# Optimization experiments

Measured on AMD Instinct MI355X. Metric: run time of the kernel, lower is better.

Reference implementation:

```python
import jax, jax.numpy as jnp
import numpy as np

DIM = 768
NUM_HEADS = 12
DECAY_RATE = 5.0


def setup_inputs() -> dict:
    key = jax.random.key(0)
    k1, k2, k3, k4 = jax.random.split(key, 4)
    B, N, C = 4, 1024, DIM
    x = jax.random.normal(k1, (B, N, C), dtype=jnp.float32)
    # torch nn.Linear weights: y = x @ W.T ; qkv_bias=False
    qkv_w = jax.random.normal(k2, (3 * C, C), dtype=jnp.float32) * (1.0 / np.sqrt(C))
    proj_w = jax.random.normal(k3, (C, C), dtype=jnp.float32) * (1.0 / np.sqrt(C))
    proj_b = jax.random.normal(k4, (C,), dtype=jnp.float32) * 0.01
    return {"x": x, "qkv_w": qkv_w, "proj_w": proj_w, "proj_b": proj_b, "cur_epoch": 3}


def reference(x, qkv_w, proj_w, proj_b, cur_epoch):
    B, N, C = x.shape
    H = NUM_HEADS
    hd = C // H
    scale = hd ** -0.5

    qkv = (x @ qkv_w.T).reshape(B, N, 3, H, hd).transpose(2, 0, 3, 1, 4)  # [3,B,H,N,hd]
    q, k, v = qkv[0], qkv[1], qkv[2]

    scores = jnp.einsum("bhqd,bhkd->bhqk", q, k) * scale
    logp = jax.nn.log_softmax(scores, axis=-1)
    attn = jnp.exp(logp)  # [B,H,N,N]

    # Per-key entropy: column j of attn flattened over (B,H,N) is renormalized
    # by Categorical; dividing by num_heads cancels under normalization.
    # H(p/s) = log(s) - (1/s) * sum(p * log p)
    s = jnp.sum(attn, axis=(0, 1, 2))                 # [N]
    plogp = jnp.sum(attn * logp, axis=(0, 1, 2))      # [N]
    entropies = jnp.log(s) - plogp / s

    # threshold decay: factor = sum_{i=0}^{cur_epoch-1} decay*exp(-(i+1))
    factor = DECAY_RATE * float(np.sum(np.exp(-(np.arange(cur_epoch) + 1.0))))
    entropy_threshold = float(np.log(C)) - factor

    # attn[:,:,:,keep] @ v[:,:,keep,:] == (attn * mask) @ v  (zeroed columns drop out)
    mask = (entropies <= entropy_threshold).astype(attn.dtype)  # [N]
    out = jnp.einsum("bhqk,bhkd->bhqd", attn * mask[None, None, None, :], v)
    out = out.transpose(0, 2, 1, 3).reshape(B, N, C)
    out = out @ proj_w.T + proj_b
    return out
```

## Files before the change

kernel.cpp:

```cpp
#include <hip/hip_runtime.h>


typedef __bf16 bf16x8 __attribute__((ext_vector_type(8)));
typedef __bf16 bf16x4 __attribute__((ext_vector_type(4)));
typedef float  f32x4  __attribute__((ext_vector_type(4)));

#define MFMA16(a, b, c) __builtin_amdgcn_mfma_f32_16x16x32_bf16((a), (b), (c), 0, 0, 0)
#define QSCALE 0.18033688f
#define LN2    0.69314718f

__device__ __forceinline__ void ld_glds16(const __bf16* g, __bf16* s) {
  __builtin_amdgcn_global_load_lds(
      (const __attribute__((address_space(1))) unsigned int*)g,
      (__attribute__((address_space(3))) unsigned int*)s, 16, 0, 0);
}

__global__ __launch_bounds__(256) void kc_conv(
    const float* __restrict__ x, const float* __restrict__ qw, const float* __restrict__ pw,
    __bf16* __restrict__ xb, __bf16* __restrict__ qwb, __bf16* __restrict__ pwb,
    float* __restrict__ colSP, int* __restrict__ keepCnt)
{
  const int i = blockIdx.x * 256 + threadIdx.x;
  const float4* src;
  __bf16* dst;
  int j;
  if (i < 786432)       { src = (const float4*)x;  dst = xb;  j = i; }
  else if (i < 1228800) { src = (const float4*)qw; dst = qwb; j = i - 786432; }
  else                  { src = (const float4*)pw; dst = pwb; j = i - 1228800; }
  const float4 f = src[j];
  bf16x4 o;
  o[0] = (__bf16)f.x; o[1] = (__bf16)f.y; o[2] = (__bf16)f.z; o[3] = (__bf16)f.w;
  *(bf16x4*)(dst + 4 * (size_t)j) = o;
  if (i < 2048) colSP[i] = 0.f;
  if (i == 0) *keepCnt = 0;
}

__global__ __launch_bounds__(256) void kg_qkv(
    const __bf16* __restrict__ A, const __bf16* __restrict__ Bm,
    __bf16* __restrict__ qb, __bf16* __restrict__ kb, float* __restrict__ v)
{
  __shared__ __bf16 As[128 * 64];
  __shared__ __bf16 Bs[128 * 64];
  const int tid = threadIdx.x;
  const int w = tid >> 6, lane = tid & 63, quad = lane >> 4, l = lane & 15;
  const int wm = w >> 1, wn = w & 1;
  const int r0 = blockIdx.y * 128, c0 = blockIdx.x * 128;
  const int srow = lane >> 3, skk = (lane & 7) * 8;

  f32x4 acc[4][4] = {};

  for (int k0 = 0; k0 < 768; k0 += 64) {
    if (k0) __syncthreads();
#pragma unroll
    for (int s = 0; s < 4; ++s) {
      const int si = w * 4 + s;
      const int row = si * 8 + srow;
      ld_glds16(A + (size_t)(r0 + row) * 768 + k0 + skk, &As[si * 512]);
      ld_glds16(Bm + (size_t)(c0 + row) * 768 + k0 + skk, &Bs[si * 512]);
    }
    __syncthreads();
#pragma unroll
    for (int kk = 0; kk < 2; ++kk) {
      bf16x8 af[4], bf[4];
#pragma unroll
      for (int t = 0; t < 4; ++t) {
        af[t] = *(const bf16x8*)&As[(wm * 64 + t * 16 + l) * 64 + kk * 32 + quad * 8];
        bf[t] = *(const bf16x8*)&Bs[(wn * 64 + t * 16 + l) * 64 + kk * 32 + quad * 8];
      }
#pragma unroll
      for (int mt = 0; mt < 4; ++mt)
#pragma unroll
        for (int nt = 0; nt < 4; ++nt)
          acc[mt][nt] = MFMA16(af[mt], bf[nt], acc[mt][nt]);
    }
  }

  const int part = c0 / 768;
  const int cbase = c0 % 768;
#pragma unroll
  for (int mt = 0; mt < 4; ++mt) {
#pragma unroll
    for (int nt = 0; nt < 4; ++nt) {
      const int cc = cbase + wn * 64 + nt * 16 + l;
      const int h = cc >> 6, d = cc & 63;
#pragma unroll
      for (int i = 0; i < 4; ++i) {
        const int rg = r0 + wm * 64 + mt * 16 + quad * 4 + i;
        const int b_ = rg >> 10, n = rg & 1023;
        const size_t off = ((size_t)(b_ * 12 + h) * 1024 + n) * 64 + d;
        const float val = acc[mt][nt][i];
        if (part == 0)      qb[off] = (__bf16)(val * QSCALE);
        else if (part == 1) kb[off] = (__bf16)val;
        else                v[off]  = val;
      }
    }
  }
}

__global__ __launch_bounds__(512) void ks_fused(
    const __bf16* __restrict__ qb, const __bf16* __restrict__ kb,
    float* __restrict__ lse, float* __restrict__ colSP)
{
  __shared__ float sS[1024];
  __shared__ float sP[1024];
  __shared__ float zrow[64];
  const int tid = threadIdx.x;
  const int w = tid >> 6, lane = tid & 63, quad = lane >> 4, l = lane & 15;
  const int bh = blockIdx.x, r0 = blockIdx.y * 64;
  for (int i = tid; i < 1024; i += 512) { sS[i] = 0.f; sP[i] = 0.f; }
  if (tid < 64) zrow[tid] = 0.f;
  __syncthreads();

  const __bf16* qbase = qb + ((size_t)bh * 1024 + r0 + l) * 64;
  bf16x8 aq0[4], aq1[4];
#pragma unroll
  for (int rt = 0; rt < 4; ++rt) {
    aq0[rt] = *(const bf16x8*)(qbase + rt * 1024 + quad * 8);
    aq1[rt] = *(const bf16x8*)(qbase + rt * 1024 + 32 + quad * 8);
  }
  const __bf16* kfrag = kb + (size_t)bh * 65536 + (size_t)(w * 16 + l) * 64 + quad * 8;
  const f32x4 zero = {0.f, 0.f, 0.f, 0.f};

  bf16x8 kf0 = *(const bf16x8*)(kfrag);
  bf16x8 kf1 = *(const bf16x8*)(kfrag + 32);

  float z[16] = {};
  for (int s = 0; s < 8; ++s) {
    const bf16x8 c0 = kf0, c1 = kf1;
    const int nxt = (s + 1) & 7;
    kf0 = *(const bf16x8*)(kfrag + (size_t)nxt * 8192);
    kf1 = *(const bf16x8*)(kfrag + (size_t)nxt * 8192 + 32);
    f32x4 av[4];
#pragma unroll
    for (int rt = 0; rt < 4; ++rt) {
      av[rt] = MFMA16(aq0[rt], c0, zero);
      av[rt] = MFMA16(aq1[rt], c1, av[rt]);
    }
#pragma unroll
    for (int rt = 0; rt < 4; ++rt)
#pragma unroll
      for (int r = 0; r < 4; ++r) z[rt * 4 + r] += exp2f(av[rt][r]);
  }
#pragma unroll
  for (int off = 1; off < 16; off <<= 1) {
#pragma unroll
    for (int i = 0; i < 16; ++i) z[i] += __shfl_xor(z[i], off);
  }
  if (l == 0) {
#pragma unroll
    for (int rt = 0; rt < 4; ++rt)
#pragma unroll
      for (int r = 0; r < 4; ++r)
        atomicAdd(&zrow[rt * 16 + quad * 4 + r], z[rt * 4 + r]);
  }
  __syncthreads();
  if (tid < 64) lse[bh * 1024 + r0 + tid] = __log2f(zrow[tid]);
  float nlb[16];
#pragma unroll
  for (int rt = 0; rt < 4; ++rt)
#pragma unroll
    for (int r = 0; r < 4; ++r)
      nlb[rt * 4 + r] = -__log2f(zrow[rt * 16 + quad * 4 + r]);

  for (int s = 0; s < 8; ++s) {
    const bf16x8 c0 = kf0, c1 = kf1;
    if (s < 7) {
      kf0 = *(const bf16x8*)(kfrag + (size_t)(s + 1) * 8192);
      kf1 = *(const bf16x8*)(kfrag + (size_t)(s + 1) * 8192 + 32);
    }
    f32x4 av[4];
#pragma unroll
    for (int rt = 0; rt < 4; ++rt) {
      av[rt] = MFMA16(aq0[rt], c0, zero);
      av[rt] = MFMA16(aq1[rt], c1, av[rt]);
    }
    float cs = 0.f, cp = 0.f;
#pragma unroll
    for (int rt = 0; rt < 4; ++rt) {
#pragma unroll
      for (int r = 0; r < 4; ++r) {
        const float d = av[rt][r] + nlb[rt * 4 + r];
        const float t = exp2f(d);
        cs += t;
        cp = fmaf(t, d, cp);
      }
    }
    cs += __shfl_xor(cs, 16); cs += __shfl_xor(cs, 32);
    cp += __shfl_xor(cp, 16); cp += __shfl_xor(cp, 32);
    if (lane < 16) {
      sS[s * 128 + w * 16 + l] += cs;
      sP[s * 128 + w * 16 + l] += cp;
    }
  }
  __syncthreads();
  for (int i = tid; i < 1024; i += 512) {
    atomicAdd(&colSP[i], sS[i]);
    atomicAdd(&colSP[1024 + i], sP[i]);
  }
}

__global__ void k_mask(const float* __restrict__ colSP, const int* __restrict__ cur_epoch,
                       float* __restrict__ mask, int* __restrict__ keepCnt)
{
  const int j = threadIdx.x;
  const float s = colSP[j];
  const float plogp = colSP[1024 + j] * LN2;
  const float ent = __logf(s) - plogp / s;
  const int ce = cur_epoch[0];
  float factor = 0.f;
  for (int i = 1; i <= ce; ++i) factor += __expf(-(float)i);
  factor *= 5.0f;
  const float thr = __logf(768.0f) - factor;
  const int keep = (ent <= thr) ? 1 : 0;
  mask[j] = keep ? 1.0f : 0.0f;
  if (keep) atomicAdd(keepCnt, 1);
}

__global__ __launch_bounds__(256) void k_av(
    const __bf16* __restrict__ qb, const __bf16* __restrict__ kb,
    const float* __restrict__ v, const float* __restrict__ lse,
    const float* __restrict__ mask, const int* __restrict__ keepCnt,
    __bf16* __restrict__ ctxb)
{
  if (*keepCnt == 0) return;
  const int tid = threadIdx.x;
  const int bh = blockIdx.x, r0 = blockIdx.y * 32;
  const int b_ = bh / 12, h = bh % 12;
  __shared__ float qs[32][64];
  __shared__ float pbuf[4][8][64];
  for (int i = tid; i < 2048; i += 256)
    qs[i >> 6][i & 63] = (float)qb[((size_t)bh * 1024 + r0) * 64 + i];
  __syncthreads();
  const int w = tid >> 6, l = tid & 63, rb = w * 8;
  float ls[8];
#pragma unroll
  for (int i = 0; i < 8; ++i) ls[i] = lse[bh * 1024 + r0 + rb + i];
  float acc[8] = {};
  for (int chunk = 0; chunk < 16; ++chunk) {
    const float mk = mask[chunk * 64 + l];
    if (__ballot(mk != 0.0f) == 0ull) continue;
    const __bf16* kp = kb + ((size_t)bh * 1024 + chunk * 64 + l) * 64;
    float s[8] = {};
    for (int d0 = 0; d0 < 64; d0 += 8) {
      const bf16x8 kf = *(const bf16x8*)(kp + d0);
#pragma unroll
      for (int dd = 0; dd < 8; ++dd) {
        const float kv = (float)kf[dd];
#pragma unroll
        for (int i = 0; i < 8; ++i) s[i] += qs[rb + i][d0 + dd] * kv;
      }
    }
    __syncthreads();
#pragma unroll
    for (int i = 0; i < 8; ++i)
      pbuf[w][i][l] = exp2f(s[i] - ls[i]) * mk;
    __syncthreads();
    const float* vp = v + ((size_t)bh * 1024 + chunk * 64) * 64 + l;
    for (int jj = 0; jj < 64; ++jj) {
      const float vv = vp[(size_t)jj * 64];
#pragma unroll
      for (int i = 0; i < 8; ++i) acc[i] += pbuf[w][i][jj] * vv;
    }
  }
#pragma unroll
  for (int i = 0; i < 8; ++i)
    ctxb[((size_t)(b_ * 1024 + r0 + rb + i)) * 768 + h * 64 + l] = (__bf16)acc[i];
}

__global__ __launch_bounds__(256) void kg_proj(
    const __bf16* __restrict__ A, const __bf16* __restrict__ Bm,
    const float* __restrict__ bias, const int* __restrict__ keepCnt,
    float* __restrict__ out)
{
  const int tid = threadIdx.x;
  const int w = tid >> 6, lane = tid & 63, quad = lane >> 4, l = lane & 15;
  const int r0 = blockIdx.y * 64, c0 = blockIdx.x * 64;
  if (*keepCnt == 0) {
#pragma unroll
    for (int ct = 0; ct < 4; ++ct) {
      const int c = c0 + ct * 16 + l;
      const float bv = bias[c];
#pragma unroll
      for (int i = 0; i < 4; ++i) {
        const int rg = r0 + w * 16 + quad * 4 + i;
        out[(size_t)rg * 768 + c] = bv;
      }
    }
    return;
  }
  __shared__ __bf16 As[64 * 72];
  __shared__ __bf16 Bs[64 * 72];
  const int row = tid >> 3, ko = (tid & 7) * 8;
  const f32x4 zero = {0.f, 0.f, 0.f, 0.f};
  f32x4 acc[4];
#pragma unroll
  for (int ct = 0; ct < 4; ++ct) acc[ct] = zero;

  uint4 a0 = *(const uint4*)(A + (size_t)(r0 + row) * 768 + ko);
  uint4 a1 = *(const uint4*)(A + (size_t)(r0 + row + 32) * 768 + ko);
  uint4 b0 = *(const uint4*)(Bm + (size_t)(c0 + row) * 768 + ko);
  uint4 b1 = *(const uint4*)(Bm + (size_t)(c0 + row + 32) * 768 + ko);

  for (int k0 = 0; k0 < 768; k0 += 64) {
    __syncthreads();
    *(uint4*)&As[row * 72 + ko] = a0;
    *(uint4*)&As[(row + 32) * 72 + ko] = a1;
    *(uint4*)&Bs[row * 72 + ko] = b0;
    *(uint4*)&Bs[(row + 32) * 72 + ko] = b1;
    __syncthreads();
    if (k0 < 704) {
      a0 = *(const uint4*)(A + (size_t)(r0 + row) * 768 + k0 + 64 + ko);
      a1 = *(const uint4*)(A + (size_t)(r0 + row + 32) * 768 + k0 + 64 + ko);
      b0 = *(const uint4*)(Bm + (size_t)(c0 + row) * 768 + k0 + 64 + ko);
      b1 = *(const uint4*)(Bm + (size_t)(c0 + row + 32) * 768 + k0 + 64 + ko);
    }
    const bf16x8 af0 = *(const bf16x8*)&As[(w * 16 + l) * 72 + quad * 8];
    const bf16x8 af1 = *(const bf16x8*)&As[(w * 16 + l) * 72 + 32 + quad * 8];
#pragma unroll
    for (int ct = 0; ct < 4; ++ct) {
      const bf16x8 bf0 = *(const bf16x8*)&Bs[(ct * 16 + l) * 72 + quad * 8];
      const bf16x8 bf1 = *(const bf16x8*)&Bs[(ct * 16 + l) * 72 + 32 + quad * 8];
      acc[ct] = MFMA16(af0, bf0, acc[ct]);
      acc[ct] = MFMA16(af1, bf1, acc[ct]);
    }
  }
#pragma unroll
  for (int ct = 0; ct < 4; ++ct) {
    const int c = c0 + ct * 16 + l;
#pragma unroll
    for (int i = 0; i < 4; ++i) {
      const int rg = r0 + w * 16 + quad * 4 + i;
      out[(size_t)rg * 768 + c] = acc[ct][i] + bias[c];
    }
  }
}

extern "C" void kernel_launch(void* const* d_in, const int* in_sizes, int n_in,
                              void* d_out, int out_size, void* d_ws, size_t ws_size,
                              hipStream_t stream)
{
  const float* x      = (const float*)d_in[0];
  const float* qkv_w  = (const float*)d_in[1];
  const float* proj_w = (const float*)d_in[2];
  const float* proj_b = (const float*)d_in[3];
  const int*   cur_ep = (const int*)d_in[4];

  char* W = (char*)d_ws;
  __bf16* xb    = (__bf16*)(W + 0);
  __bf16* qwb   = (__bf16*)(W + 6291456);
  __bf16* pwb   = (__bf16*)(W + 9830400);
  __bf16* qb    = (__bf16*)(W + 11010048);
  __bf16* kb    = (__bf16*)(W + 17301504);
  float*  v     = (float*) (W + 23592960);
  __bf16* ctxb  = (__bf16*)(W + 36175872);
  float*  lse   = (float*) (W + 42467328);
  float*  mask  = (float*) (W + 42663936);
  int*    keep  = (int*)   (W + 42668032);
  float*  colSP = (float*) (W + 42668544);
  float*  out   = (float*)d_out;

  kc_conv<<<5376, 256, 0, stream>>>(x, qkv_w, proj_w, xb, qwb, pwb, colSP, keep);
  kg_qkv<<<dim3(18, 32), 256, 0, stream>>>(xb, qwb, qb, kb, v);
  ks_fused<<<dim3(48, 16), 512, 0, stream>>>(qb, kb, lse, colSP);
  k_mask<<<1, 1024, 0, stream>>>(colSP, cur_ep, mask, keep);
  k_av<<<dim3(48, 32), 256, 0, stream>>>(qb, kb, v, lse, mask, keep, ctxb);
  kg_proj<<<dim3(12, 64), 256, 0, stream>>>(ctxb, pwb, proj_b, keep, out);
}
```

Measured before the change: 157.8 us.

## Restructure score kernel to hold K tiles in registers with smaller row blocks

The column-statistics kernel now processes 32 query rows per block instead of 64. Each wave loads its 128 keys' K fragments into registers once and reuses them for both the row-sum pass and the column-stat pass, replacing the streamed K reloads. The shared-memory column accumulators and their sync are replaced by per-lane column accumulators that are atomically added straight to global memory. exp2f is swapped for the hardware exp2 builtin in both score kernels. The trade-off is twice as many blocks (and twice the QK work per key, since K is loaded per 32 rows), more global atomics, and higher register pressure.

After: 163.5 us. 1.04x slower.

```diff
diff --git a/kernel.cpp b/kernel.cpp
--- a/kernel.cpp
+++ b/kernel.cpp
@@ -8,6 +8,12 @@
 #define MFMA16(a, b, c) __builtin_amdgcn_mfma_f32_16x16x32_bf16((a), (b), (c), 0, 0, 0)
 #define QSCALE 0.18033688f
 #define LN2    0.69314718f
+
+#if __has_builtin(__builtin_amdgcn_exp2f)
+#define EXP2(x) __builtin_amdgcn_exp2f(x)
+#else
+#define EXP2(x) exp2f(x)
+#endif
 
 __device__ __forceinline__ void ld_glds16(const __bf16* g, __bf16* s) {
   __builtin_amdgcn_global_load_lds(
@@ -101,101 +107,88 @@
     const __bf16* __restrict__ qb, const __bf16* __restrict__ kb,
     float* __restrict__ lse, float* __restrict__ colSP)
 {
-  __shared__ float sS[1024];
-  __shared__ float sP[1024];
-  __shared__ float zrow[64];
+  __shared__ float zrow[32];
   const int tid = threadIdx.x;
   const int w = tid >> 6, lane = tid & 63, quad = lane >> 4, l = lane & 15;
-  const int bh = blockIdx.x, r0 = blockIdx.y * 64;
-  for (int i = tid; i < 1024; i += 512) { sS[i] = 0.f; sP[i] = 0.f; }
-  if (tid < 64) zrow[tid] = 0.f;
+  const int bh = blockIdx.x, r0 = blockIdx.y * 32;
+  if (tid < 32) zrow[tid] = 0.f;
   __syncthreads();
 
   const __bf16* qbase = qb + ((size_t)bh * 1024 + r0 + l) * 64;
-  bf16x8 aq0[4], aq1[4];
-#pragma unroll
-  for (int rt = 0; rt < 4; ++rt) {
+  bf16x8 aq0[2], aq1[2];
+#pragma unroll
+  for (int rt = 0; rt < 2; ++rt) {
     aq0[rt] = *(const bf16x8*)(qbase + rt * 1024 + quad * 8);
     aq1[rt] = *(const bf16x8*)(qbase + rt * 1024 + 32 + quad * 8);
   }
-  const __bf16* kfrag = kb + (size_t)bh * 65536 + (size_t)(w * 16 + l) * 64 + quad * 8;
+  const __bf16* kbase = kb + (size_t)bh * 65536 + (size_t)(w * 128 + l) * 64 + quad * 8;
+  bf16x8 kc0[8], kc1[8];
+#pragma unroll
+  for (int ct = 0; ct < 8; ++ct) {
+    kc0[ct] = *(const bf16x8*)(kbase + ct * 1024);
+    kc1[ct] = *(const bf16x8*)(kbase + ct * 1024 + 32);
+  }
   const f32x4 zero = {0.f, 0.f, 0.f, 0.f};
 
-  bf16x8 kf0 = *(const bf16x8*)(kfrag);
-  bf16x8 kf1 = *(const bf16x8*)(kfrag + 32);
-
-  float z[16] = {};
-  for (int s = 0; s < 8; ++s) {
-    const bf16x8 c0 = kf0, c1 = kf1;
-    const int nxt = (s + 1) & 7;
-    kf0 = *(const bf16x8*)(kfrag + (size_t)nxt * 8192);
-    kf1 = *(const bf16x8*)(kfrag + (size_t)nxt * 8192 + 32);
-    f32x4 av[4];
-#pragma unroll
-    for (int rt = 0; rt < 4; ++rt) {
-      av[rt] = MFMA16(aq0[rt], c0, zero);
-      av[rt] = MFMA16(aq1[rt], c1, av[rt]);
-    }
-#pragma unroll
-    for (int rt = 0; rt < 4; ++rt)
-#pragma unroll
-      for (int r = 0; r < 4; ++r) z[rt * 4 + r] += exp2f(av[rt][r]);
+  float z[8] = {};
+#pragma unroll
+  for (int ct = 0; ct < 8; ++ct) {
+#pragma unroll
+    for (int rt = 0; rt < 2; ++rt) {
+      f32x4 av = MFMA16(aq0[rt], kc0[ct], zero);
+      av = MFMA16(aq1[rt], kc1[ct], av);
+#pragma unroll
+      for (int r = 0; r < 4; ++r) z[rt * 4 + r] += EXP2(av[r]);
+    }
   }
 #pragma unroll
   for (int off = 1; off < 16; off <<= 1) {
 #pragma unroll
-    for (int i = 0; i < 16; ++i) z[i] += __shfl_xor(z[i], off);
+    for (int i = 0; i < 8; ++i) z[i] += __shfl_xor(z[i], off);
   }
   if (l == 0) {
 #pragma unroll
-    for (int rt = 0; rt < 4; ++rt)
+    for (int rt = 0; rt < 2; ++rt)
 #pragma unroll
       for (int r = 0; r < 4; ++r)
         atomicAdd(&zrow[rt * 16 + quad * 4 + r], z[rt * 4 + r]);
   }
   __syncthreads();
-  if (tid < 64) lse[bh * 1024 + r0 + tid] = __log2f(zrow[tid]);
-  float nlb[16];
-#pragma unroll
-  for (int rt = 0; rt < 4; ++rt)
+  if (tid < 32) lse[bh * 1024 + r0 + tid] = __log2f(zrow[tid]);
+  float nlb[8];
+#pragma unroll
+  for (int rt = 0; rt < 2; ++rt)
 #pragma unroll
     for (int r = 0; r < 4; ++r)
       nlb[rt * 4 + r] = -__log2f(zrow[rt * 16 + quad * 4 + r]);
 
-  for (int s = 0; s < 8; ++s) {
-    const bf16x8 c0 = kf0, c1 = kf1;
-    if (s < 7) {
-      kf0 = *(const bf16x8*)(kfrag + (size_t)(s + 1) * 8192);
-      kf1 = *(const bf16x8*)(kfrag + (size_t)(s + 1) * 8192 + 32);
-    }
-    f32x4 av[4];
-#pragma unroll
-    for (int rt = 0; rt < 4; ++rt) {
-      av[rt] = MFMA16(aq0[rt], c0, zero);
-      av[rt] = MFMA16(aq1[rt], c1, av[rt]);
-    }
-    float cs = 0.f, cp = 0.f;
-#pragma unroll
-    for (int rt = 0; rt < 4; ++rt) {
+  float cs[8] = {}, cp[8] = {};
+#pragma unroll
+  for (int rt = 0; rt < 2; ++rt) {
+#pragma unroll
+    for (int ct = 0; ct < 8; ++ct) {
+      f32x4 av = MFMA16(aq0[rt], kc0[ct], zero);
+      av = MFMA16(aq1[rt], kc1[ct], av);
 #pragma unroll
       for (int r = 0; r < 4; ++r) {
-        const float d = av[rt][r] + nlb[rt * 4 + r];
-        const float t = exp2f(d);
-        cs += t;
-        cp = fmaf(t, d, cp);
-      }
-    }
-    cs += __shfl_xor(cs, 16); cs += __shfl_xor(cs, 32);
-    cp += __shfl_xor(cp, 16); cp += __shfl_xor(cp, 32);
-    if (lane < 16) {
-      sS[s * 128 + w * 16 + l] += cs;
-      sP[s * 128 + w * 16 + l] += cp;
-    }
-  }
-  __syncthreads();
-  for (int i = tid; i < 1024; i += 512) {
-    atomicAdd(&colSP[i], sS[i]);
-    atomicAdd(&colSP[1024 + i], sP[i]);
+        const float d = av[r] + nlb[rt * 4 + r];
+        const float t = EXP2(d);
+        cs[ct] += t;
+        cp[ct] = fmaf(t, d, cp[ct]);
+      }
+    }
+  }
+#pragma unroll
+  for (int ct = 0; ct < 8; ++ct) {
+    cs[ct] += __shfl_xor(cs[ct], 16); cs[ct] += __shfl_xor(cs[ct], 32);
+    cp[ct] += __shfl_xor(cp[ct], 16); cp[ct] += __shfl_xor(cp[ct], 32);
+  }
+  if (lane < 16) {
+#pragma unroll
+    for (int ct = 0; ct < 8; ++ct) {
+      atomicAdd(&colSP[w * 128 + ct * 16 + l], cs[ct]);
+      atomicAdd(&colSP[1024 + w * 128 + ct * 16 + l], cp[ct]);
+    }
   }
 }
 
@@ -253,7 +246,7 @@
     __syncthreads();
 #pragma unroll
     for (int i = 0; i < 8; ++i)
-      pbuf[w][i][l] = exp2f(s[i] - ls[i]) * mk;
+      pbuf[w][i][l] = EXP2(s[i] - ls[i]) * mk;
     __syncthreads();
     const float* vp = v + ((size_t)bh * 1024 + chunk * 64) * 64 + l;
     for (int jj = 0; jj < 64; ++jj) {
@@ -361,7 +354,7 @@
 
   kc_conv<<<5376, 256, 0, stream>>>(x, qkv_w, proj_w, xb, qwb, pwb, colSP, keep);
   kg_qkv<<<dim3(18, 32), 256, 0, stream>>>(xb, qwb, qb, kb, v);
-  ks_fused<<<dim3(48, 16), 512, 0, stream>>>(qb, kb, lse, colSP);
+  ks_fused<<<dim3(48, 32), 512, 0, stream>>>(qb, kb, lse, colSP);
   k_mask<<<1, 1024, 0, stream>>>(colSP, cur_ep, mask, keep);
   k_av<<<dim3(48, 32), 256, 0, stream>>>(qb, kb, v, lse, mask, keep, ctxb);
   kg_proj<<<dim3(12, 64), 256, 0, stream>>>(ctxb, pwb, proj_b, keep, out);
```

## Fuse mask computation into score kernel via last-block pattern and double-buffer QK

Applied to the files above, without the earlier changes.

Drops the separate single-block mask kernel by having the last finishing ks_fused block, detected through an atomic done counter, compute entropies and the keep mask. Both score passes are restructured into a two-stage software pipeline that computes the next chunk's MFMA while the exp2 work of the previous chunk runs. exp2f is replaced by the hardware exp2 builtin throughout. This saves one launch and exposes more overlap, at the cost of extra registers, a threadfence, and a serial tail executed by one block.

New measurement: 234.4 us. 48.6% more time.

```diff
diff --git a/kernel.cpp b/kernel.cpp
--- a/kernel.cpp
+++ b/kernel.cpp
@@ -8,6 +8,12 @@
 #define MFMA16(a, b, c) __builtin_amdgcn_mfma_f32_16x16x32_bf16((a), (b), (c), 0, 0, 0)
 #define QSCALE 0.18033688f
 #define LN2    0.69314718f
+
+#if __has_builtin(__builtin_amdgcn_exp2f)
+#define EXP2(x) __builtin_amdgcn_exp2f(x)
+#else
+#define EXP2(x) exp2f(x)
+#endif
 
 __device__ __forceinline__ void ld_glds16(const __bf16* g, __bf16* s) {
   __builtin_amdgcn_global_load_lds(
@@ -18,7 +24,7 @@
 __global__ __launch_bounds__(256) void kc_conv(
     const float* __restrict__ x, const float* __restrict__ qw, const float* __restrict__ pw,
     __bf16* __restrict__ xb, __bf16* __restrict__ qwb, __bf16* __restrict__ pwb,
-    float* __restrict__ colSP, int* __restrict__ keepCnt)
+    float* __restrict__ colSP, int* __restrict__ keepCnt, unsigned int* __restrict__ done)
 {
   const int i = blockIdx.x * 256 + threadIdx.x;
   const float4* src;
@@ -32,7 +38,7 @@
   o[0] = (__bf16)f.x; o[1] = (__bf16)f.y; o[2] = (__bf16)f.z; o[3] = (__bf16)f.w;
   *(bf16x4*)(dst + 4 * (size_t)j) = o;
   if (i < 2048) colSP[i] = 0.f;
-  if (i == 0) *keepCnt = 0;
+  if (i == 0) { *keepCnt = 0; *done = 0u; }
 }
 
 __global__ __launch_bounds__(256) void kg_qkv(
@@ -97,13 +103,26 @@
   }
 }
 
+__device__ __forceinline__ void qk2(const bf16x8* aq0, const bf16x8* aq1,
+                                    bf16x8 k0, bf16x8 k1, f32x4* av) {
+  const f32x4 zero = {0.f, 0.f, 0.f, 0.f};
+#pragma unroll
+  for (int rt = 0; rt < 4; ++rt) {
+    av[rt] = MFMA16(aq0[rt], k0, zero);
+    av[rt] = MFMA16(aq1[rt], k1, av[rt]);
+  }
+}
+
 __global__ __launch_bounds__(512) void ks_fused(
     const __bf16* __restrict__ qb, const __bf16* __restrict__ kb,
-    float* __restrict__ lse, float* __restrict__ colSP)
+    float* __restrict__ lse, float* __restrict__ colSP,
+    const int* __restrict__ cur_epoch, float* __restrict__ mask,
+    int* __restrict__ keepCnt, unsigned int* __restrict__ done)
 {
   __shared__ float sS[1024];
   __shared__ float sP[1024];
   __shared__ float zrow[64];
+  __shared__ int lastBlk;
   const int tid = threadIdx.x;
   const int w = tid >> 6, lane = tid & 63, quad = lane >> 4, l = lane & 15;
   const int bh = blockIdx.x, r0 = blockIdx.y * 64;
@@ -119,28 +138,41 @@
     aq1[rt] = *(const bf16x8*)(qbase + rt * 1024 + 32 + quad * 8);
   }
   const __bf16* kfrag = kb + (size_t)bh * 65536 + (size_t)(w * 16 + l) * 64 + quad * 8;
-  const f32x4 zero = {0.f, 0.f, 0.f, 0.f};
-
-  bf16x8 kf0 = *(const bf16x8*)(kfrag);
-  bf16x8 kf1 = *(const bf16x8*)(kfrag + 32);
+
+  bf16x8 ka0, ka1, kb0, kb1;
+  f32x4 avA[4], avB[4];
+  ka0 = *(const bf16x8*)(kfrag);
+  ka1 = *(const bf16x8*)(kfrag + 32);
+  kb0 = *(const bf16x8*)(kfrag + 8192);
+  kb1 = *(const bf16x8*)(kfrag + 8192 + 32);
+  qk2(aq0, aq1, ka0, ka1, avA);
 
   float z[16] = {};
-  for (int s = 0; s < 8; ++s) {
-    const bf16x8 c0 = kf0, c1 = kf1;
-    const int nxt = (s + 1) & 7;
-    kf0 = *(const bf16x8*)(kfrag + (size_t)nxt * 8192);
-    kf1 = *(const bf16x8*)(kfrag + (size_t)nxt * 8192 + 32);
-    f32x4 av[4];
-#pragma unroll
-    for (int rt = 0; rt < 4; ++rt) {
-      av[rt] = MFMA16(aq0[rt], c0, zero);
-      av[rt] = MFMA16(aq1[rt], c1, av[rt]);
-    }
-#pragma unroll
-    for (int rt = 0; rt < 4; ++rt)
-#pragma unroll
-      for (int r = 0; r < 4; ++r) z[rt * 4 + r] += exp2f(av[rt][r]);
-  }
+#pragma unroll
+  for (int s2 = 0; s2 < 4; ++s2) {
+    const int s = 2 * s2;
+    {
+      const int c = (s + 2) & 7;
+      ka0 = *(const bf16x8*)(kfrag + (size_t)c * 8192);
+      ka1 = *(const bf16x8*)(kfrag + (size_t)c * 8192 + 32);
+      qk2(aq0, aq1, kb0, kb1, avB);
+#pragma unroll
+      for (int rt = 0; rt < 4; ++rt)
+#pragma unroll
+        for (int r = 0; r < 4; ++r) z[rt * 4 + r] += EXP2(avA[rt][r]);
+    }
+    {
+      const int c = (s + 3) & 7;
+      kb0 = *(const bf16x8*)(kfrag + (size_t)c * 8192);
+      kb1 = *(const bf16x8*)(kfrag + (size_t)c * 8192 + 32);
+      qk2(aq0, aq1, ka0, ka1, avA);
+#pragma unroll
+      for (int rt = 0; rt < 4; ++rt)
+#pragma unroll
+        for (int r = 0; r < 4; ++r) z[rt * 4 + r] += EXP2(avB[rt][r]);
+    }
+  }
+
 #pragma unroll
   for (int off = 1; off < 16; off <<= 1) {
 #pragma unroll
@@ -162,25 +194,14 @@
     for (int r = 0; r < 4; ++r)
       nlb[rt * 4 + r] = -__log2f(zrow[rt * 16 + quad * 4 + r]);
 
-  for (int s = 0; s < 8; ++s) {
-    const bf16x8 c0 = kf0, c1 = kf1;
-    if (s < 7) {
-      kf0 = *(const bf16x8*)(kfrag + (size_t)(s + 1) * 8192);
-      kf1 = *(const bf16x8*)(kfrag + (size_t)(s + 1) * 8192 + 32);
-    }
-    f32x4 av[4];
-#pragma unroll
-    for (int rt = 0; rt < 4; ++rt) {
-      av[rt] = MFMA16(aq0[rt], c0, zero);
-      av[rt] = MFMA16(aq1[rt], c1, av[rt]);
-    }
+  auto consume2 = [&](const f32x4* av, int s) {
     float cs = 0.f, cp = 0.f;
 #pragma unroll
     for (int rt = 0; rt < 4; ++rt) {
 #pragma unroll
       for (int r = 0; r < 4; ++r) {
         const float d = av[rt][r] + nlb[rt * 4 + r];
-        const float t = exp2f(d);
+        const float t = EXP2(d);
         cs += t;
         cp = fmaf(t, d, cp);
       }
@@ -191,29 +212,48 @@
       sS[s * 128 + w * 16 + l] += cs;
       sP[s * 128 + w * 16 + l] += cp;
     }
+  };
+#pragma unroll
+  for (int s2 = 0; s2 < 4; ++s2) {
+    const int s = 2 * s2;
+    {
+      const int c = (s + 2) & 7;
+      ka0 = *(const bf16x8*)(kfrag + (size_t)c * 8192);
+      ka1 = *(const bf16x8*)(kfrag + (size_t)c * 8192 + 32);
+      qk2(aq0, aq1, kb0, kb1, avB);
+      consume2(avA, s);
+    }
+    {
+      const int c = (s + 3) & 7;
+      kb0 = *(const bf16x8*)(kfrag + (size_t)c * 8192);
+      kb1 = *(const bf16x8*)(kfrag + (size_t)c * 8192 + 32);
+      qk2(aq0, aq1, ka0, ka1, avA);
+      consume2(avB, s + 1);
+    }
   }
   __syncthreads();
   for (int i = tid; i < 1024; i += 512) {
     atomicAdd(&colSP[i], sS[i]);
     atomicAdd(&colSP[1024 + i], sP[i]);
   }
-}
-
-__global__ void k_mask(const float* __restrict__ colSP, const int* __restrict__ cur_epoch,
-                       float* __restrict__ mask, int* __restrict__ keepCnt)
-{
-  const int j = threadIdx.x;
-  const float s = colSP[j];
-  const float plogp = colSP[1024 + j] * LN2;
-  const float ent = __logf(s) - plogp / s;
-  const int ce = cur_epoch[0];
-  float factor = 0.f;
-  for (int i = 1; i <= ce; ++i) factor += __expf(-(float)i);
-  factor *= 5.0f;
-  const float thr = __logf(768.0f) - factor;
-  const int keep = (ent <= thr) ? 1 : 0;
-  mask[j] = keep ? 1.0f : 0.0f;
-  if (keep) atomicAdd(keepCnt, 1);
+
+  __threadfence();
+  if (tid == 0) lastBlk = (atomicAdd(done, 1u) == 767u) ? 1 : 0;
+  __syncthreads();
+  if (!lastBlk) return;
+  for (int j = tid; j < 1024; j += 512) {
+    const float s  = __hip_atomic_load(&colSP[j], __ATOMIC_RELAXED, __HIP_MEMORY_SCOPE_AGENT);
+    const float pl = __hip_atomic_load(&colSP[1024 + j], __ATOMIC_RELAXED, __HIP_MEMORY_SCOPE_AGENT) * LN2;
+    const float ent = __logf(s) - pl / s;
+    const int ce = cur_epoch[0];
+    float factor = 0.f;
+    for (int i = 1; i <= ce; ++i) factor += __expf(-(float)i);
+    factor *= 5.0f;
+    const float thr = __logf(768.0f) - factor;
+    const int keep = (ent <= thr) ? 1 : 0;
+    mask[j] = keep ? 1.0f : 0.0f;
+    if (keep) atomicAdd(keepCnt, 1);
+  }
 }
 
 __global__ __launch_bounds__(256) void k_av(
@@ -253,7 +293,7 @@
     __syncthreads();
 #pragma unroll
     for (int i = 0; i < 8; ++i)
-      pbuf[w][i][l] = exp2f(s[i] - ls[i]) * mk;
+      pbuf[w][i][l] = EXP2(s[i] - ls[i]) * mk;
     __syncthreads();
     const float* vp = v + ((size_t)bh * 1024 + chunk * 64) * 64 + l;
     for (int jj = 0; jj < 64; ++jj) {
@@ -356,13 +396,13 @@
   float*  lse   = (float*) (W + 42467328);
   float*  mask  = (float*) (W + 42663936);
   int*    keep  = (int*)   (W + 42668032);
+  unsigned int* done = (unsigned int*)(W + 42668036);
   float*  colSP = (float*) (W + 42668544);
   float*  out   = (float*)d_out;
 
-  kc_conv<<<5376, 256, 0, stream>>>(x, qkv_w, proj_w, xb, qwb, pwb, colSP, keep);
+  kc_conv<<<5376, 256, 0, stream>>>(x, qkv_w, proj_w, xb, qwb, pwb, colSP, keep, done);
   kg_qkv<<<dim3(18, 32), 256, 0, stream>>>(xb, qwb, qb, kb, v);
-  ks_fused<<<dim3(48, 16), 512, 0, stream>>>(qb, kb, lse, colSP);
-  k_mask<<<1, 1024, 0, stream>>>(colSP, cur_ep, mask, keep);
+  ks_fused<<<dim3(48, 16), 512, 0, stream>>>(qb, kb, lse, colSP, cur_ep, mask, keep, done);
   k_av<<<dim3(48, 32), 256, 0, stream>>>(qb, kb, v, lse, mask, keep, ctxb);
   kg_proj<<<dim3(12, 64), 256, 0, stream>>>(ctxb, pwb, proj_b, keep, out);
 }
```
